# Optimization experiments

Measured on AMD Instinct MI355X. Metric: run time of the kernel, lower is better.

Reference implementation:

```python
import jax, jax.numpy as jnp
import numpy as np

N = 100_000   # nodes
E = 6_400_000  # edges (avg degree 64)
K = 3          # TAGConv hops -> K+1 linear terms per layer


def setup_inputs() -> dict:
    key = jax.random.key(0)
    ks = jax.random.split(key, 9)
    return {
        "x": jax.random.normal(ks[0], (N,), jnp.float32),
        "edge_index": jax.random.randint(ks[1], (2, E), 0, N, jnp.int32),
        "edge_attr": jax.random.normal(ks[2], (E,), jnp.float32),
        "k": 5000,
        "W1": jax.random.normal(ks[3], (K + 1, 1, 8), jnp.float32) * 0.5,
        "b1": jax.random.normal(ks[4], (8,), jnp.float32) * 0.1,
        "W2": jax.random.normal(ks[5], (K + 1, 8, 8), jnp.float32) * 0.2,
        "b2": jax.random.normal(ks[6], (8,), jnp.float32) * 0.1,
        "W3": jax.random.normal(ks[7], (K + 1, 8, 1), jnp.float32) * 0.2,
        "b3": jax.random.normal(ks[8], (1,), jnp.float32) * 0.1,
    }


def _gcn_norm(src, dst, edge_weight, num_nodes):
    # PyG gcn_norm with add_self_loops=False: deg over target index,
    # norm_e = d^{-1/2}[src] * w_e * d^{-1/2}[dst]
    deg = jax.ops.segment_sum(edge_weight, dst, num_segments=num_nodes)
    dis = jnp.where(deg > 0, jax.lax.rsqrt(jnp.where(deg > 0, deg, 1.0)), 0.0)
    return dis[src] * edge_weight * dis[dst]


def _tagconv(x, W, b, src, dst, norm, num_nodes):
    # out = sum_{h=0..K} (A_norm^h x) @ W[h] + b
    out = x @ W[0]
    h = x
    for i in range(1, W.shape[0]):
        h = jax.ops.segment_sum(norm[:, None] * h[src], dst, num_segments=num_nodes)
        out = out + h @ W[i]
    return out + b


def reference(x, edge_index, edge_attr, k, W1, b1, W2, b2, W3, b3):
    num_nodes = x.shape[0]
    x = x[:, None]  # [N, 1]
    src, dst = edge_index[0], edge_index[1]
    norm = _gcn_norm(src, dst, jnp.abs(edge_attr), num_nodes)

    x = jax.nn.relu(_tagconv(x, W1, b1, src, dst, norm, num_nodes))
    x = jax.nn.relu(_tagconv(x, W2, b2, src, dst, norm, num_nodes))
    x = jax.nn.relu(_tagconv(x, W3, b3, src, dst, norm, num_nodes))

    # tg.nn.InstanceNorm(1), batch=None, affine=False: normalize over all nodes
    mean = jnp.mean(x)
    var = jnp.mean((x - mean) ** 2)
    x = ((x - mean) * jax.lax.rsqrt(var + 1e-5)).squeeze(-1)  # [N]

    # top-k one-hot mask (argsort descending -> first k indices)
    _, top_idx = jax.lax.top_k(x, k)
    top_vec = jnp.zeros_like(x).at[top_idx].set(1.0)
    return jnp.column_stack((x, top_vec))  # [N, 2]
```

## Files before the change

### kernel.cpp

```cpp
#include <hip/hip_runtime.h>

#define BS 256
#define BSB 512
#define BSF 1024
#define GPN 16
#define NBLKB 1024
#define BSH 8
#define SMAX 400

static __device__ __forceinline__ float relu_(float v) { return fmaxf(v, 0.0f); }


__global__ void k_binhist(const int* __restrict__ dst, int* __restrict__ bcnt,
                          int E, int chunk, int nbuck) {
  __shared__ int h[1024];
  int b = blockIdx.x, t = threadIdx.x;
  for (int i = t; i < nbuck; i += BSB) h[i] = 0;
  __syncthreads();
  int beg = b * chunk, end = min(E, beg + chunk);
  for (int e = beg + t; e < end; e += BSB) atomicAdd(&h[dst[e] >> BSH], 1);
  __syncthreads();
  for (int i = t; i < nbuck; i += BSB) bcnt[(size_t)i * NBLKB + b] = h[i];
}

__global__ void k_bucketscan(int* __restrict__ bcnt, int* __restrict__ btot) {
  __shared__ int sh[BS];
  int bkt = blockIdx.x, t = threadIdx.x;
  size_t base = (size_t)bkt * NBLKB;
  int c[4], s = 0;
#pragma unroll
  for (int j = 0; j < 4; ++j) { c[j] = bcnt[base + t * 4 + j]; s += c[j]; }
  sh[t] = s; __syncthreads();
  for (int off = 1; off < BS; off <<= 1) {
    int add = (t >= off) ? sh[t - off] : 0; __syncthreads();
    sh[t] += add; __syncthreads();
  }
  int run = sh[t] - s;
#pragma unroll
  for (int j = 0; j < 4; ++j) { bcnt[base + t * 4 + j] = run; run += c[j]; }
  if (t == BS - 1) btot[bkt] = run;
}

__global__ void k_basescan(const int* __restrict__ btot, int* __restrict__ bbase, int nbuck) {
  __shared__ int sh[BS];
  int t = threadIdx.x;
  int run = 0;
  for (int c = 0; c < nbuck; c += BS) {
    int i = c + t;
    int v = (i < nbuck) ? btot[i] : 0;
    sh[t] = v; __syncthreads();
    for (int off = 1; off < BS; off <<= 1) {
      int add = (t >= off) ? sh[t - off] : 0; __syncthreads();
      sh[t] += add; __syncthreads();
    }
    if (i < nbuck) bbase[i] = run + sh[t] - v;
    run += sh[BS - 1];
    __syncthreads();
  }
}

__global__ void k_bin(const int* __restrict__ src, const int* __restrict__ dst,
                      const float* __restrict__ attr, const int* __restrict__ bcnt,
                      const int* __restrict__ bbase, int2* __restrict__ bed,
                      int E, int chunk, int nbuck) {
  __shared__ int2 stage[SMAX][9];
  __shared__ int  fc[SMAX];
  __shared__ int  cur[SMAX];
  int b = blockIdx.x, t = threadIdx.x;
  for (int i = t; i < nbuck; i += BSB) {
    cur[i] = bbase[i] + bcnt[(size_t)i * NBLKB + b];
    fc[i] = 0;
  }
  __syncthreads();
  int beg = b * chunk, end = min(E, beg + chunk);
  for (int base = beg; base < end; base += BSB) {
    int e = base + t;
    if (e < end) {
      int d = dst[e];
      int bkt = d >> BSH;
      int2 rec = make_int2((int)(((unsigned)(d & ((1 << BSH) - 1)) << 17) | (unsigned)src[e]),
                           __float_as_int(fabsf(attr[e])));
      int slot = atomicAdd(&fc[bkt], 1);
      if (slot < 8) stage[bkt][slot] = rec;
      else { int gp = atomicAdd(&cur[bkt], 1); bed[gp] = rec; }
    }
    __syncthreads();
    for (int i = t; i < nbuck; i += BSB) {
      int c = fc[i]; if (c > 8) c = 8;
      if (c == 8) {
        int gp = cur[i]; cur[i] = gp + 8;
#pragma unroll
        for (int j = 0; j < 8; ++j) bed[gp + j] = stage[i][j];
        fc[i] = 0;
      }
    }
    __syncthreads();
  }
  for (int i = t; i < nbuck; i += BSB) {
    int c = fc[i]; if (c > 8) c = 8;
    if (c) {
      int gp = cur[i];
      for (int j = 0; j < c; ++j) bed[gp + j] = stage[i][j];
    }
  }
}

__global__ void k_cntfill(const int2* __restrict__ bed, const int* __restrict__ bbase,
                          const int* __restrict__ btot, const float* __restrict__ x,
                          float* __restrict__ dis, float* __restrict__ xhat,
                          int* __restrict__ rowptr, int2* __restrict__ adj, int N, int E) {
  __shared__ int   lc[1 << BSH];
  __shared__ float ld[1 << BSH];
  __shared__ int   sc[1 << BSH];
  __shared__ int   rcur[1 << BSH];
  int bkt = blockIdx.x, t = threadIdx.x;
  if (t < (1 << BSH)) { lc[t] = 0; ld[t] = 0.f; }
  __syncthreads();
  int beg = bbase[bkt], tot = btot[bkt];
  for (int i = t; i < tot; i += BSF) {
    int2 rec = bed[beg + i];
    int dl = (int)((unsigned)rec.x >> 17);
    atomicAdd(&lc[dl], 1);
    atomicAdd(&ld[dl], __int_as_float(rec.y));
  }
  __syncthreads();
  if (t < (1 << BSH)) sc[t] = lc[t];
  __syncthreads();
  for (int off = 1; off < (1 << BSH); off <<= 1) {
    int add = 0;
    if (t < (1 << BSH) && t >= off) add = sc[t - off];
    __syncthreads();
    if (t < (1 << BSH)) sc[t] += add;
    __syncthreads();
  }
  if (t < (1 << BSH)) {
    int myrow = beg + sc[t] - lc[t];
    rcur[t] = myrow;
    int n = (bkt << BSH) + t;
    if (n < N) {
      rowptr[n] = myrow;
      float dg = ld[t];
      float d = (dg > 0.f) ? (1.0f / sqrtf(dg)) : 0.f;
      dis[n] = d;
      xhat[n] = d * x[n];
    }
  }
  if (bkt == (int)gridDim.x - 1 && t == 0) rowptr[N] = E;
  __syncthreads();
  for (int i = t; i < tot; i += BSF) {
    int2 rec = bed[beg + i];
    unsigned u = (unsigned)rec.x;
    int dl = (int)(u >> 17);
    int pos = atomicAdd(&rcur[dl], 1);
    adj[pos] = make_int2((int)(u & 0x1FFFFu), rec.y);
  }
}


__global__ void k_scanA(const int* __restrict__ cnt, int* __restrict__ bsum, int N) {
  __shared__ int sh[BS];
  int t = threadIdx.x;
  int base = blockIdx.x * 1024;
  int s = 0;
#pragma unroll
  for (int j = 0; j < 4; ++j) { int i = base + t * 4 + j; s += (i < N) ? cnt[i] : 0; }
  sh[t] = s; __syncthreads();
  for (int off = 128; off; off >>= 1) { if (t < off) sh[t] += sh[t + off]; __syncthreads(); }
  if (t == 0) bsum[blockIdx.x] = sh[0];
}

__global__ void k_scanB(int* __restrict__ bsum, int NB2) {
  __shared__ int sh[BS];
  int t = threadIdx.x;
  int v = (t < NB2) ? bsum[t] : 0;
  sh[t] = v; __syncthreads();
  for (int off = 1; off < BS; off <<= 1) {
    int add = (t >= off) ? sh[t - off] : 0; __syncthreads();
    sh[t] += add; __syncthreads();
  }
  if (t < NB2) bsum[t] = sh[t] - v;
}

__global__ void k_scanC(const int* __restrict__ cnt, const int* __restrict__ bsum,
                        int* __restrict__ rowptr, int* __restrict__ cursor, int N, int E) {
  __shared__ int sh[BS];
  int b = blockIdx.x, t = threadIdx.x;
  int base = b * 1024;
  int c[4]; int s = 0;
#pragma unroll
  for (int j = 0; j < 4; ++j) { int i = base + t * 4 + j; c[j] = (i < N) ? cnt[i] : 0; s += c[j]; }
  sh[t] = s; __syncthreads();
  for (int off = 1; off < BS; off <<= 1) {
    int add = (t >= off) ? sh[t - off] : 0; __syncthreads();
    sh[t] += add; __syncthreads();
  }
  int run = sh[t] - s + bsum[b];
#pragma unroll
  for (int j = 0; j < 4; ++j) {
    int i = base + t * 4 + j;
    if (i < N) { rowptr[i] = run; if (cursor) cursor[i] = run; run += c[j]; }
  }
  if (b == 0 && t == 0) rowptr[N] = E;
}

__global__ void k_count(const int* __restrict__ dst, int* __restrict__ cnt, int E) {
  int e = blockIdx.x * blockDim.x + threadIdx.x;
  if (e < E) atomicAdd(&cnt[dst[e]], 1);
}

__global__ void k_place(const int* __restrict__ src, const int* __restrict__ dst,
                        const float* __restrict__ attr, int* __restrict__ cursor,
                        int2* __restrict__ adj, int E) {
  int e = blockIdx.x * blockDim.x + threadIdx.x;
  if (e >= E) return;
  int d = dst[e];
  int pos = atomicAdd(&cursor[d], 1);
  adj[pos] = make_int2(src[e], __float_as_int(fabsf(attr[e])));
}

__global__ void k_degdis(const int* __restrict__ rowptr, const int2* __restrict__ adj,
                         const float* __restrict__ x, float* __restrict__ dis,
                         float* __restrict__ xhat, int N) {
  int g = (blockIdx.x * blockDim.x + threadIdx.x) / GPN;
  int l = threadIdx.x & (GPN - 1);
  if (g >= N) return;
  int beg = rowptr[g], end = rowptr[g + 1];
  float s = 0.0f;
  for (int e = beg + l; e < end; e += GPN) s += __int_as_float(adj[e].y);
#pragma unroll
  for (int off = 8; off; off >>= 1) s += __shfl_xor(s, off, GPN);
  if (l == 0) {
    float d = (s > 0.0f) ? (1.0f / sqrtf(s)) : 0.0f;
    dis[g] = d;
    xhat[g] = d * x[g];
  }
}


static __device__ __forceinline__ float edge_sum1(const int2* __restrict__ adj,
                                                  const float* __restrict__ uin,
                                                  int beg, int end, int l) {
  float a0 = 0.f, a1 = 0.f, a2 = 0.f, a3 = 0.f;
  int e = beg + l;
  for (; e + 3 * GPN < end; e += 4 * GPN) {
    int2 s0 = adj[e], s1 = adj[e + GPN], s2 = adj[e + 2 * GPN], s3 = adj[e + 3 * GPN];
    a0 += __int_as_float(s0.y) * uin[s0.x];
    a1 += __int_as_float(s1.y) * uin[s1.x];
    a2 += __int_as_float(s2.y) * uin[s2.x];
    a3 += __int_as_float(s3.y) * uin[s3.x];
  }
  for (; e < end; e += GPN) { int2 s0 = adj[e]; a0 += __int_as_float(s0.y) * uin[s0.x]; }
  float acc = (a0 + a1) + (a2 + a3);
#pragma unroll
  for (int off = 8; off; off >>= 1) acc += __shfl_xor(acc, off, GPN);
  return acc;
}

__global__ void k_gp1_uh(const int* __restrict__ rowptr, const int2* __restrict__ adj,
                         const float* __restrict__ uin, const float* __restrict__ dis,
                         float* __restrict__ hout, float* __restrict__ uout, int N) {
  int g = (blockIdx.x * blockDim.x + threadIdx.x) / GPN;
  int l = threadIdx.x & (GPN - 1);
  if (g >= N) return;
  float acc = edge_sum1(adj, uin, rowptr[g], rowptr[g + 1], l);
  if (l == 0) {
    float d = dis[g];
    float h = d * acc;
    hout[g] = h;
    uout[g] = d * h;
  }
}

__global__ void k_gp1_y(const int* __restrict__ rowptr, const int2* __restrict__ adj,
                        const float* __restrict__ u2, const float* __restrict__ x,
                        const float* __restrict__ h1, const float* __restrict__ h2,
                        const float* __restrict__ dis, const float* __restrict__ W1,
                        const float* __restrict__ b1, const float* __restrict__ W23,
                        float* __restrict__ y, float* __restrict__ Phat, int N) {
  int g = (blockIdx.x * blockDim.x + threadIdx.x) / GPN;
  int l = threadIdx.x & (GPN - 1);
  if (g >= N) return;
  float acc = edge_sum1(adj, u2, rowptr[g], rowptr[g + 1], l);
  if (l == 0) {
    float d = dis[g];
    float xv = x[g], a = h1[g], b = h2[g], c = d * acc;
    float o[8];
#pragma unroll
    for (int j = 0; j < 8; ++j)
      o[j] = relu_(xv * W1[j] + a * W1[8 + j] + b * W1[16 + j] + c * W1[24 + j] + b1[j]);
    float4* op = (float4*)(y + (size_t)g * 8);
    op[0] = make_float4(o[0], o[1], o[2], o[3]);
    op[1] = make_float4(o[4], o[5], o[6], o[7]);
    float p[8];
#pragma unroll
    for (int j = 0; j < 8; ++j) {
      float s = 0.0f;
#pragma unroll
      for (int i = 0; i < 8; ++i) s += o[i] * W23[i * 8 + j];
      p[j] = d * s;
    }
    float4* pp = (float4*)(Phat + (size_t)g * 8);
    pp[0] = make_float4(p[0], p[1], p[2], p[3]);
    pp[1] = make_float4(p[4], p[5], p[6], p[7]);
  }
}

#define EDGE_SUM8(ADJ, UIN, BEG, END, L)                                        \
  float a0=0,a1=0,a2=0,a3=0,a4=0,a5=0,a6=0,a7=0;                                \
  {                                                                             \
    int e = (BEG) + (L);                                                        \
    int last = (END) - GPN;                                                     \
    for (; e < last; e += 2 * GPN) {                                            \
      int2 s0 = (ADJ)[e], s1 = (ADJ)[e + GPN];                                  \
      float w0 = __int_as_float(s0.y), w1 = __int_as_float(s1.y);               \
      const float4* p0 = (const float4*)((UIN) + (size_t)s0.x * 8);             \
      const float4* p1 = (const float4*)((UIN) + (size_t)s1.x * 8);             \
      float4 u0 = p0[0], v0 = p0[1], u1 = p1[0], v1 = p1[1];                    \
      a0 += w0*u0.x; a1 += w0*u0.y; a2 += w0*u0.z; a3 += w0*u0.w;               \
      a4 += w0*v0.x; a5 += w0*v0.y; a6 += w0*v0.z; a7 += w0*v0.w;               \
      a0 += w1*u1.x; a1 += w1*u1.y; a2 += w1*u1.z; a3 += w1*u1.w;               \
      a4 += w1*v1.x; a5 += w1*v1.y; a6 += w1*v1.z; a7 += w1*v1.w;               \
    }                                                                           \
    if (e < (END)) {                                                            \
      int2 s0 = (ADJ)[e];                                                       \
      float w0 = __int_as_float(s0.y);                                          \
      const float4* p0 = (const float4*)((UIN) + (size_t)s0.x * 8);             \
      float4 u0 = p0[0], v0 = p0[1];                                            \
      a0 += w0*u0.x; a1 += w0*u0.y; a2 += w0*u0.z; a3 += w0*u0.w;               \
      a4 += w0*v0.x; a5 += w0*v0.y; a6 += w0*v0.z; a7 += w0*v0.w;               \
    }                                                                           \
  }                                                                             \
  _Pragma("unroll")                                                             \
  for (int off = 8; off; off >>= 1) {                                           \
    a0 += __shfl_xor(a0, off, GPN); a1 += __shfl_xor(a1, off, GPN);             \
    a2 += __shfl_xor(a2, off, GPN); a3 += __shfl_xor(a3, off, GPN);             \
    a4 += __shfl_xor(a4, off, GPN); a5 += __shfl_xor(a5, off, GPN);             \
    a6 += __shfl_xor(a6, off, GPN); a7 += __shfl_xor(a7, off, GPN);             \
  }

__global__ void k_gp8_u(const int* __restrict__ rowptr, const int2* __restrict__ adj,
                        const float* __restrict__ uin, const float* __restrict__ y,
                        const float* __restrict__ W, const float* __restrict__ dis,
                        float* __restrict__ uout, int N) {
  int g = (blockIdx.x * blockDim.x + threadIdx.x) / GPN;
  int l = threadIdx.x & (GPN - 1);
  if (g >= N) return;
  int beg = rowptr[g], end = rowptr[g + 1];
  EDGE_SUM8(adj, uin, beg, end, l)
  if (l == 0) {
    float d = dis[g];
    const float4* yp = (const float4*)(y + (size_t)g * 8);
    float4 u = yp[0], v = yp[1];
    float yi[8] = {u.x, u.y, u.z, u.w, v.x, v.y, v.z, v.w};
    float acc[8] = {a0, a1, a2, a3, a4, a5, a6, a7};
    float o[8];
#pragma unroll
    for (int j = 0; j < 8; ++j) {
      float s = 0.0f;
#pragma unroll
      for (int i = 0; i < 8; ++i) s += yi[i] * W[i * 8 + j];
      o[j] = d * (s + d * acc[j]);
    }
    float4* op = (float4*)(uout + (size_t)g * 8);
    op[0] = make_float4(o[0], o[1], o[2], o[3]);
    op[1] = make_float4(o[4], o[5], o[6], o[7]);
  }
}

__global__ void k_gp8_fin(const int* __restrict__ rowptr, const int2* __restrict__ adj,
                          const float* __restrict__ uin, const float* __restrict__ y,
                          const float* __restrict__ W0, const float* __restrict__ b2,
                          const float* __restrict__ W3, const float* __restrict__ dis,
                          float* __restrict__ S3hat, float* __restrict__ B2,
                          float* __restrict__ B1, float* __restrict__ B0, int N) {
  int g = (blockIdx.x * blockDim.x + threadIdx.x) / GPN;
  int l = threadIdx.x & (GPN - 1);
  if (g >= N) return;
  int beg = rowptr[g], end = rowptr[g + 1];
  EDGE_SUM8(adj, uin, beg, end, l)
  if (l == 0) {
    float d = dis[g];
    const float4* yp = (const float4*)(y + (size_t)g * 8);
    float4 u = yp[0], v = yp[1];
    float yi[8] = {u.x, u.y, u.z, u.w, v.x, v.y, v.z, v.w};
    float acc[8] = {a0, a1, a2, a3, a4, a5, a6, a7};
    float z[8];
#pragma unroll
    for (int j = 0; j < 8; ++j) {
      float s = 0.0f;
#pragma unroll
      for (int i = 0; i < 8; ++i) s += yi[i] * W0[i * 8 + j];
      z[j] = relu_(s + d * acc[j] + b2[j]);
    }
    float tt[4];
#pragma unroll
    for (int i = 0; i < 4; ++i) {
      float s = 0.0f;
#pragma unroll
      for (int j = 0; j < 8; ++j) s += z[j] * W3[i * 8 + j];
      tt[i] = s;
    }
    B0[g] = tt[0]; B1[g] = tt[1]; B2[g] = tt[2];
    S3hat[g] = d * tt[3];
  }
}

__global__ void k_gp1_bu(const int* __restrict__ rowptr, const int2* __restrict__ adj,
                         const float* __restrict__ uin, const float* __restrict__ B,
                         const float* __restrict__ dis, float* __restrict__ uout, int N) {
  int g = (blockIdx.x * blockDim.x + threadIdx.x) / GPN;
  int l = threadIdx.x & (GPN - 1);
  if (g >= N) return;
  float acc = edge_sum1(adj, uin, rowptr[g], rowptr[g + 1], l);
  if (l == 0) {
    float d = dis[g];
    uout[g] = d * (B[g] + d * acc);
  }
}

__global__ void k_gp1_last(const int* __restrict__ rowptr, const int2* __restrict__ adj,
                           const float* __restrict__ uin, const float* __restrict__ B0,
                           const float* __restrict__ b3, const float* __restrict__ dis,
                           float* __restrict__ r, unsigned* __restrict__ keys,
                           double* __restrict__ partials, int N) {
  __shared__ double s1[BS];
  __shared__ double s2[BS];
  int tid = blockIdx.x * blockDim.x + threadIdx.x;
  int g = tid / GPN, l = tid & (GPN - 1);
  float rv = 0.0f;
  bool writer = false;
  if (g < N) {
    float acc = edge_sum1(adj, uin, rowptr[g], rowptr[g + 1], l);
    if (l == 0) {
      float gg = B0[g] + dis[g] * acc;
      rv = relu_(gg + b3[0]);
      r[g] = rv;
      keys[g] = __float_as_uint(rv) | 0x80000000u;
      writer = true;
    }
  }
  double v = writer ? (double)rv : 0.0;
  s1[threadIdx.x] = v;
  s2[threadIdx.x] = v * v;
  __syncthreads();
  for (int off = 128; off; off >>= 1) {
    if (threadIdx.x < off) {
      s1[threadIdx.x] += s1[threadIdx.x + off];
      s2[threadIdx.x] += s2[threadIdx.x + off];
    }
    __syncthreads();
  }
  if (threadIdx.x == 0) {
    partials[2 * (size_t)blockIdx.x]     = s1[0];
    partials[2 * (size_t)blockIdx.x + 1] = s2[0];
  }
}

__global__ void k_stats(const double* __restrict__ partials, int nparts,
                        float* __restrict__ stats, unsigned* __restrict__ state,
                        const int* __restrict__ kp, int N) {
  __shared__ double s1[BS];
  __shared__ double s2[BS];
  int t = threadIdx.x;
  double a = 0.0, b = 0.0;
  for (int i = t; i < nparts; i += BS) { a += partials[2 * (size_t)i]; b += partials[2 * (size_t)i + 1]; }
  s1[t] = a; s2[t] = b;
  __syncthreads();
  for (int off = 128; off; off >>= 1) {
    if (t < off) { s1[t] += s1[t + off]; s2[t] += s2[t + off]; }
    __syncthreads();
  }
  if (t == 0) {
    double mean = s1[0] / (double)N;
    double var  = s2[0] / (double)N - mean * mean;
    stats[0] = (float)mean;
    stats[1] = (float)(1.0 / sqrt(var + 1e-5));
    state[0] = 0u;
    state[1] = (unsigned)kp[0];
  }
}


__global__ void k_hist(const unsigned* __restrict__ keys, int N,
                       const unsigned* __restrict__ state, unsigned* __restrict__ hist,
                       int shift) {
  __shared__ unsigned sh[256];
  sh[threadIdx.x] = 0;
  __syncthreads();
  unsigned prefix = state[0];
  unsigned hmask = (shift >= 24) ? 0u : (0xFFFFFFFFu << (shift + 8));
  int stride = gridDim.x * blockDim.x;
  for (int n = blockIdx.x * blockDim.x + threadIdx.x; n < N; n += stride) {
    unsigned kk = keys[n];
    if ((kk & hmask) == (prefix & hmask)) atomicAdd(&sh[(kk >> shift) & 255u], 1u);
  }
  __syncthreads();
  atomicAdd(&hist[threadIdx.x], sh[threadIdx.x]);
}

__global__ void k_select(unsigned* __restrict__ state, unsigned* __restrict__ hist, int shift) {
  __shared__ unsigned sh[BS];
  int t = threadIdx.x;
  unsigned c = hist[t];
  sh[t] = c;
  __syncthreads();
  for (int off = 1; off < BS; off <<= 1) {
    unsigned add = (t + off < BS) ? sh[t + off] : 0u; __syncthreads();
    sh[t] += add; __syncthreads();
  }
  unsigned rem = state[1];
  unsigned S = sh[t];
  if (S >= rem && (S - c) < rem) {
    state[0] |= ((unsigned)t) << shift;
    state[1] = rem - (S - c);
  }
  hist[t] = 0;
}

__global__ void k_mark(const unsigned* __restrict__ keys, const float* __restrict__ r,
                       const float* __restrict__ stats, int N,
                       const unsigned* __restrict__ state, float* __restrict__ out,
                       unsigned* __restrict__ blkcnt) {
  unsigned T = state[0];
  float mean = stats[0], istd = stats[1];
  int n = blockIdx.x * 256 + threadIdx.x;
  int eq = 0;
  __shared__ int sh;
  if (threadIdx.x == 0) sh = 0;
  __syncthreads();
  if (n < N) {
    out[2 * (size_t)n] = (r[n] - mean) * istd;
    unsigned kk = keys[n];
    out[2 * (size_t)n + 1] = (kk > T) ? 1.0f : 0.0f;
    eq = (kk == T);
  }
  if (eq) atomicAdd(&sh, 1);
  __syncthreads();
  if (threadIdx.x == 0) blkcnt[blockIdx.x] = (unsigned)sh;
}

__global__ void k_scanP(const unsigned* __restrict__ blkcnt, unsigned* __restrict__ scanbuf, int NB) {
  __shared__ unsigned sh[BS];
  int t = threadIdx.x;
  unsigned c0 = (2 * t < NB) ? blkcnt[2 * t] : 0u;
  unsigned c1 = (2 * t + 1 < NB) ? blkcnt[2 * t + 1] : 0u;
  unsigned s = c0 + c1;
  sh[t] = s; __syncthreads();
  for (int off = 1; off < BS; off <<= 1) {
    unsigned add = (t >= off) ? sh[t - off] : 0u; __syncthreads();
    sh[t] += add; __syncthreads();
  }
  unsigned ex = sh[t] - s;
  if (2 * t < NB) scanbuf[2 * t] = ex;
  if (2 * t + 1 < NB) scanbuf[2 * t + 1] = ex + c0;
}

__global__ void k_resolve(const unsigned* __restrict__ keys, int N,
                          const unsigned* __restrict__ state,
                          const unsigned* __restrict__ scanbuf, float* __restrict__ out) {
  unsigned T = state[0];
  unsigned m = state[1];
  int n = blockIdx.x * 256 + threadIdx.x;
  if (n >= N) return;
  if (keys[n] != T) return;
  unsigned rank = scanbuf[blockIdx.x];
  int base = blockIdx.x * 256;
  for (int j = base; j < n; ++j) rank += (keys[j] == T);
  out[2 * (size_t)n + 1] = (rank < m) ? 1.0f : 0.0f;
}


extern "C" void kernel_launch(void* const* d_in, const int* in_sizes, int n_in,
                              void* d_out, int out_size, void* d_ws, size_t ws_size,
                              hipStream_t stream) {
  const float* x    = (const float*)d_in[0];
  const int*   ei   = (const int*)d_in[1];
  const float* attr = (const float*)d_in[2];
  const int*   kp   = (const int*)d_in[3];
  const float* W1   = (const float*)d_in[4];
  const float* b1   = (const float*)d_in[5];
  const float* W2   = (const float*)d_in[6];
  const float* b2   = (const float*)d_in[7];
  const float* W3   = (const float*)d_in[8];
  const float* b3   = (const float*)d_in[9];
  const int N = in_sizes[0];
  const int E = in_sizes[2];
  const int* src = ei;
  const int* dst = ei + E;
  float* out = (float*)d_out;
  const int NB    = (N + 255) / 256;
  const int NB2   = (N + 1023) / 1024;
  const int NBUCK = (N + (1 << BSH) - 1) >> BSH;
  const int chunk = (E + NBLKB - 1) / NBLKB;
  const int GGB   = (int)(((size_t)N * GPN + BS - 1) / BS);

  char* p = (char*)d_ws;
  auto alloc = [&](size_t bytes) -> char* {
    char* r = p; p += (bytes + 255) & ~(size_t)255; return r;
  };
  float*    dis    = (float*)alloc((size_t)N * 4);
  float*    xhat   = (float*)alloc((size_t)N * 4);
  float*    h1     = (float*)alloc((size_t)N * 4);
  float*    h2     = (float*)alloc((size_t)N * 4);
  float*    u1     = (float*)alloc((size_t)N * 4);
  float*    u2     = (float*)alloc((size_t)N * 4);
  float*    y      = (float*)alloc((size_t)N * 32);
  float*    Phat   = (float*)alloc((size_t)N * 32);
  float*    Qhat   = (float*)alloc((size_t)N * 32);
  float*    S3hat  = (float*)alloc((size_t)N * 4);
  float*    B2     = (float*)alloc((size_t)N * 4);
  float*    B1     = (float*)alloc((size_t)N * 4);
  float*    B0     = (float*)alloc((size_t)N * 4);
  float*    g2hat  = (float*)alloc((size_t)N * 4);
  float*    g1hat  = (float*)alloc((size_t)N * 4);
  float*    r      = (float*)alloc((size_t)N * 4);
  unsigned* keys   = (unsigned*)alloc((size_t)N * 4);
  double*   parts  = (double*)alloc((size_t)GGB * 16);
  float*    stats  = (float*)alloc(8);
  unsigned* state  = (unsigned*)alloc(8);
  unsigned* hist   = (unsigned*)alloc(1024);
  unsigned* blkcnt = (unsigned*)alloc((size_t)NB * 4);
  unsigned* scanbf = (unsigned*)alloc((size_t)NB * 4);
  int*      rowptr = (int*)alloc((size_t)(N + 1) * 4);
  int*      cursor = (int*)alloc((size_t)N * 4);
  int*      cnt    = (int*)alloc((size_t)N * 4);
  int*      bsum   = (int*)alloc(2048);
  int2*     adj    = (int2*)alloc((size_t)E * 8);
  int2*     bed    = (int2*)alloc((size_t)E * 8);
  int*      bcnt   = (int*)alloc((size_t)NBUCK * NBLKB * 4);
  int*      btot   = (int*)alloc((size_t)NBUCK * 4 + 256);
  int*      bbase  = (int*)alloc((size_t)NBUCK * 4 + 256);
  size_t need_new = (size_t)(p - (char*)d_ws);

  dim3 B(BS);
  int genb = (E + BS - 1) / BS;
  dim3 GE(genb), GG(GGB), GN(NB), GB(NBUCK);

  bool use_new = (need_new <= ws_size) && (N <= 102400) && (NBUCK <= SMAX);

  hipMemsetAsync(hist, 0, 1024, stream);

  if (use_new) {
    k_binhist<<<dim3(NBLKB), dim3(BSB), 0, stream>>>(dst, bcnt, E, chunk, NBUCK);
    k_bucketscan<<<GB, B, 0, stream>>>(bcnt, btot);
    k_basescan<<<dim3(1), B, 0, stream>>>(btot, bbase, NBUCK);
    k_bin<<<dim3(NBLKB), dim3(BSB), 0, stream>>>(src, dst, attr, bcnt, bbase, bed, E, chunk, NBUCK);
    k_cntfill<<<GB, dim3(BSF), 0, stream>>>(bed, bbase, btot, x, dis, xhat, rowptr, adj, N, E);
  } else {
    hipMemsetAsync(cnt, 0, (size_t)N * 4, stream);
    k_count<<<GE, B, 0, stream>>>(dst, cnt, E);
    k_scanA<<<dim3(NB2), B, 0, stream>>>(cnt, bsum, N);
    k_scanB<<<dim3(1), B, 0, stream>>>(bsum, NB2);
    k_scanC<<<dim3(NB2), B, 0, stream>>>(cnt, bsum, rowptr, cursor, N, E);
    k_place<<<GE, B, 0, stream>>>(src, dst, attr, cursor, adj, E);
    k_degdis<<<GG, B, 0, stream>>>(rowptr, adj, x, dis, xhat, N);
  }

  k_gp1_uh<<<GG, B, 0, stream>>>(rowptr, adj, xhat, dis, h1, u1, N);
  k_gp1_uh<<<GG, B, 0, stream>>>(rowptr, adj, u1, dis, h2, u2, N);
  k_gp1_y<<<GG, B, 0, stream>>>(rowptr, adj, u2, x, h1, h2, dis, W1, b1, W2 + 3 * 64, y, Phat, N);

  k_gp8_u<<<GG, B, 0, stream>>>(rowptr, adj, Phat, y, W2 + 2 * 64, dis, Qhat, N);
  k_gp8_u<<<GG, B, 0, stream>>>(rowptr, adj, Qhat, y, W2 + 1 * 64, dis, Phat, N);
  k_gp8_fin<<<GG, B, 0, stream>>>(rowptr, adj, Phat, y, W2, b2, W3, dis, S3hat, B2, B1, B0, N);

  k_gp1_bu<<<GG, B, 0, stream>>>(rowptr, adj, S3hat, B2, dis, g2hat, N);
  k_gp1_bu<<<GG, B, 0, stream>>>(rowptr, adj, g2hat, B1, dis, g1hat, N);
  k_gp1_last<<<GG, B, 0, stream>>>(rowptr, adj, g1hat, B0, b3, dis, r, keys, parts, N);

  k_stats<<<dim3(1), B, 0, stream>>>(parts, GGB, stats, state, kp, N);

  for (int shift = 24; shift >= 0; shift -= 8) {
    k_hist<<<GN, B, 0, stream>>>(keys, N, state, hist, shift);
    k_select<<<dim3(1), B, 0, stream>>>(state, hist, shift);
  }
  k_mark<<<GN, B, 0, stream>>>(keys, r, stats, N, state, out, blkcnt);
  k_scanP<<<dim3(1), B, 0, stream>>>(blkcnt, scanbf, NB);
  k_resolve<<<GN, B, 0, stream>>>(keys, N, state, scanbf, out);
}
```

Baseline: 539.7 us.

## Run graph propagations directly on bucketed edge lists with shared-memory atomics

```diff
diff --git a/kernel.cpp b/kernel.cpp
--- a/kernel.cpp
+++ b/kernel.cpp
@@ -6,6 +6,7 @@
 #define GPN 16
 #define NBLKB 1024
 #define BSH 8
+#define NPB (1 << BSH)
 #define SMAX 400
 
 static __device__ __forceinline__ float relu_(float v) { return fmaxf(v, 0.0f); }
@@ -78,7 +79,7 @@
     if (e < end) {
       int d = dst[e];
       int bkt = d >> BSH;
-      int2 rec = make_int2((int)(((unsigned)(d & ((1 << BSH) - 1)) << 17) | (unsigned)src[e]),
+      int2 rec = make_int2((int)(((unsigned)(d & (NPB - 1)) << 17) | (unsigned)src[e]),
                            __float_as_int(fabsf(attr[e])));
       int slot = atomicAdd(&fc[bkt], 1);
       if (slot < 8) stage[bkt][slot] = rec;
@@ -105,54 +106,249 @@
   }
 }
 
-__global__ void k_cntfill(const int2* __restrict__ bed, const int* __restrict__ bbase,
+__global__ void kb_degdis(const int2* __restrict__ bed, const int* __restrict__ bbase,
                           const int* __restrict__ btot, const float* __restrict__ x,
-                          float* __restrict__ dis, float* __restrict__ xhat,
-                          int* __restrict__ rowptr, int2* __restrict__ adj, int N, int E) {
-  __shared__ int   lc[1 << BSH];
-  __shared__ float ld[1 << BSH];
-  __shared__ int   sc[1 << BSH];
-  __shared__ int   rcur[1 << BSH];
+                          float* __restrict__ dis, float* __restrict__ xhat, int N) {
+  __shared__ float ld[NPB];
   int bkt = blockIdx.x, t = threadIdx.x;
-  if (t < (1 << BSH)) { lc[t] = 0; ld[t] = 0.f; }
+  if (t < NPB) ld[t] = 0.f;
   __syncthreads();
   int beg = bbase[bkt], tot = btot[bkt];
   for (int i = t; i < tot; i += BSF) {
     int2 rec = bed[beg + i];
-    int dl = (int)((unsigned)rec.x >> 17);
-    atomicAdd(&lc[dl], 1);
-    atomicAdd(&ld[dl], __int_as_float(rec.y));
-  }
-  __syncthreads();
-  if (t < (1 << BSH)) sc[t] = lc[t];
-  __syncthreads();
-  for (int off = 1; off < (1 << BSH); off <<= 1) {
-    int add = 0;
-    if (t < (1 << BSH) && t >= off) add = sc[t - off];
-    __syncthreads();
-    if (t < (1 << BSH)) sc[t] += add;
-    __syncthreads();
-  }
-  if (t < (1 << BSH)) {
-    int myrow = beg + sc[t] - lc[t];
-    rcur[t] = myrow;
+    atomicAdd(&ld[(unsigned)rec.x >> 17], __int_as_float(rec.y));
+  }
+  __syncthreads();
+  if (t < NPB) {
     int n = (bkt << BSH) + t;
     if (n < N) {
-      rowptr[n] = myrow;
       float dg = ld[t];
       float d = (dg > 0.f) ? (1.0f / sqrtf(dg)) : 0.f;
       dis[n] = d;
       xhat[n] = d * x[n];
     }
   }
-  if (bkt == (int)gridDim.x - 1 && t == 0) rowptr[N] = E;
-  __syncthreads();
+}
+
+
+__global__ void kb_gp1_uh(const int2* __restrict__ bed, const int* __restrict__ bbase,
+                          const int* __restrict__ btot, const float* __restrict__ uin,
+                          const float* __restrict__ dis, float* __restrict__ hout,
+                          float* __restrict__ uout, int N) {
+  __shared__ float acc[NPB];
+  int bkt = blockIdx.x, t = threadIdx.x;
+  if (t < NPB) acc[t] = 0.f;
+  __syncthreads();
+  int beg = bbase[bkt], tot = btot[bkt];
   for (int i = t; i < tot; i += BSF) {
     int2 rec = bed[beg + i];
     unsigned u = (unsigned)rec.x;
-    int dl = (int)(u >> 17);
-    int pos = atomicAdd(&rcur[dl], 1);
-    adj[pos] = make_int2((int)(u & 0x1FFFFu), rec.y);
+    atomicAdd(&acc[u >> 17], __int_as_float(rec.y) * uin[u & 0x1FFFFu]);
+  }
+  __syncthreads();
+  if (t < NPB) {
+    int n = (bkt << BSH) + t;
+    if (n < N) {
+      float d = dis[n];
+      float h = d * acc[t];
+      hout[n] = h;
+      uout[n] = d * h;
+    }
+  }
+}
+
+__global__ void kb_gp1_y(const int2* __restrict__ bed, const int* __restrict__ bbase,
+                         const int* __restrict__ btot, const float* __restrict__ u2,
+                         const float* __restrict__ x, const float* __restrict__ h1,
+                         const float* __restrict__ h2, const float* __restrict__ dis,
+                         const float* __restrict__ W1, const float* __restrict__ b1,
+                         const float* __restrict__ W23, float* __restrict__ y,
+                         float* __restrict__ Phat, int N) {
+  __shared__ float acc[NPB];
+  int bkt = blockIdx.x, t = threadIdx.x;
+  if (t < NPB) acc[t] = 0.f;
+  __syncthreads();
+  int beg = bbase[bkt], tot = btot[bkt];
+  for (int i = t; i < tot; i += BSF) {
+    int2 rec = bed[beg + i];
+    unsigned u = (unsigned)rec.x;
+    atomicAdd(&acc[u >> 17], __int_as_float(rec.y) * u2[u & 0x1FFFFu]);
+  }
+  __syncthreads();
+  if (t < NPB) {
+    int n = (bkt << BSH) + t;
+    if (n < N) {
+      float d = dis[n];
+      float xv = x[n], a = h1[n], b = h2[n], c = d * acc[t];
+      float o[8];
+#pragma unroll
+      for (int j = 0; j < 8; ++j)
+        o[j] = relu_(xv * W1[j] + a * W1[8 + j] + b * W1[16 + j] + c * W1[24 + j] + b1[j]);
+      float4* op = (float4*)(y + (size_t)n * 8);
+      op[0] = make_float4(o[0], o[1], o[2], o[3]);
+      op[1] = make_float4(o[4], o[5], o[6], o[7]);
+      float pv[8];
+#pragma unroll
+      for (int j = 0; j < 8; ++j) {
+        float s = 0.0f;
+#pragma unroll
+        for (int i2 = 0; i2 < 8; ++i2) s += o[i2] * W23[i2 * 8 + j];
+        pv[j] = d * s;
+      }
+      float4* pp = (float4*)(Phat + (size_t)n * 8);
+      pp[0] = make_float4(pv[0], pv[1], pv[2], pv[3]);
+      pp[1] = make_float4(pv[4], pv[5], pv[6], pv[7]);
+    }
+  }
+}
+
+#define KB8_STREAM(UIN)                                                          \
+  __shared__ float acc[NPB][9];                                                  \
+  int bkt = blockIdx.x, t = threadIdx.x;                                         \
+  for (int i = t; i < NPB * 9; i += BSF) ((float*)acc)[i] = 0.f;                 \
+  __syncthreads();                                                               \
+  int beg = bbase[bkt], tot = btot[bkt];                                         \
+  for (int i = t; i < tot; i += BSF) {                                           \
+    int2 rec = bed[beg + i];                                                     \
+    unsigned u = (unsigned)rec.x;                                                \
+    int dl = (int)(u >> 17), s = (int)(u & 0x1FFFFu);                            \
+    float w = __int_as_float(rec.y);                                             \
+    const float4* hp = (const float4*)((UIN) + (size_t)s * 8);                   \
+    float4 a = hp[0], b = hp[1];                                                 \
+    atomicAdd(&acc[dl][0], w * a.x); atomicAdd(&acc[dl][1], w * a.y);            \
+    atomicAdd(&acc[dl][2], w * a.z); atomicAdd(&acc[dl][3], w * a.w);            \
+    atomicAdd(&acc[dl][4], w * b.x); atomicAdd(&acc[dl][5], w * b.y);            \
+    atomicAdd(&acc[dl][6], w * b.z); atomicAdd(&acc[dl][7], w * b.w);            \
+  }                                                                              \
+  __syncthreads();
+
+__global__ void kb_gp8_u(const int2* __restrict__ bed, const int* __restrict__ bbase,
+                         const int* __restrict__ btot, const float* __restrict__ uin,
+                         const float* __restrict__ y, const float* __restrict__ W,
+                         const float* __restrict__ dis, float* __restrict__ uout, int N) {
+  KB8_STREAM(uin)
+  if (t < NPB) {
+    int n = (bkt << BSH) + t;
+    if (n < N) {
+      float d = dis[n];
+      const float4* yp = (const float4*)(y + (size_t)n * 8);
+      float4 u = yp[0], v = yp[1];
+      float yi[8] = {u.x, u.y, u.z, u.w, v.x, v.y, v.z, v.w};
+      float o[8];
+#pragma unroll
+      for (int j = 0; j < 8; ++j) {
+        float s = 0.0f;
+#pragma unroll
+        for (int i2 = 0; i2 < 8; ++i2) s += yi[i2] * W[i2 * 8 + j];
+        o[j] = d * (s + d * acc[t][j]);
+      }
+      float4* op = (float4*)(uout + (size_t)n * 8);
+      op[0] = make_float4(o[0], o[1], o[2], o[3]);
+      op[1] = make_float4(o[4], o[5], o[6], o[7]);
+    }
+  }
+}
+
+__global__ void kb_gp8_fin(const int2* __restrict__ bed, const int* __restrict__ bbase,
+                           const int* __restrict__ btot, const float* __restrict__ uin,
+                           const float* __restrict__ y, const float* __restrict__ W0,
+                           const float* __restrict__ b2, const float* __restrict__ W3,
+                           const float* __restrict__ dis, float* __restrict__ S3hat,
+                           float* __restrict__ B2, float* __restrict__ B1,
+                           float* __restrict__ B0, int N) {
+  KB8_STREAM(uin)
+  if (t < NPB) {
+    int n = (bkt << BSH) + t;
+    if (n < N) {
+      float d = dis[n];
+      const float4* yp = (const float4*)(y + (size_t)n * 8);
+      float4 u = yp[0], v = yp[1];
+      float yi[8] = {u.x, u.y, u.z, u.w, v.x, v.y, v.z, v.w};
+      float z[8];
+#pragma unroll
+      for (int j = 0; j < 8; ++j) {
+        float s = 0.0f;
+#pragma unroll
+        for (int i2 = 0; i2 < 8; ++i2) s += yi[i2] * W0[i2 * 8 + j];
+        z[j] = relu_(s + d * acc[t][j] + b2[j]);
+      }
+      float tt[4];
+#pragma unroll
+      for (int i2 = 0; i2 < 4; ++i2) {
+        float s = 0.0f;
+#pragma unroll
+        for (int j = 0; j < 8; ++j) s += z[j] * W3[i2 * 8 + j];
+        tt[i2] = s;
+      }
+      B0[n] = tt[0]; B1[n] = tt[1]; B2[n] = tt[2];
+      S3hat[n] = d * tt[3];
+    }
+  }
+}
+
+__global__ void kb_gp1_bu(const int2* __restrict__ bed, const int* __restrict__ bbase,
+                          const int* __restrict__ btot, const float* __restrict__ uin,
+                          const float* __restrict__ B, const float* __restrict__ dis,
+                          float* __restrict__ uout, int N) {
+  __shared__ float acc[NPB];
+  int bkt = blockIdx.x, t = threadIdx.x;
+  if (t < NPB) acc[t] = 0.f;
+  __syncthreads();
+  int beg = bbase[bkt], tot = btot[bkt];
+  for (int i = t; i < tot; i += BSF) {
+    int2 rec = bed[beg + i];
+    unsigned u = (unsigned)rec.x;
+    atomicAdd(&acc[u >> 17], __int_as_float(rec.y) * uin[u & 0x1FFFFu]);
+  }
+  __syncthreads();
+  if (t < NPB) {
+    int n = (bkt << BSH) + t;
+    if (n < N) {
+      float d = dis[n];
+      uout[n] = d * (B[n] + d * acc[t]);
+    }
+  }
+}
+
+__global__ void kb_gp1_last(const int2* __restrict__ bed, const int* __restrict__ bbase,
+                            const int* __restrict__ btot, const float* __restrict__ uin,
+                            const float* __restrict__ B0, const float* __restrict__ b3,
+                            const float* __restrict__ dis, float* __restrict__ r,
+                            unsigned* __restrict__ keys, double* __restrict__ partials, int N) {
+  __shared__ float acc[NPB];
+  __shared__ double s1[BSF];
+  __shared__ double s2[BSF];
+  int bkt = blockIdx.x, t = threadIdx.x;
+  if (t < NPB) acc[t] = 0.f;
+  __syncthreads();
+  int beg = bbase[bkt], tot = btot[bkt];
+  for (int i = t; i < tot; i += BSF) {
+    int2 rec = bed[beg + i];
+    unsigned u = (unsigned)rec.x;
+    atomicAdd(&acc[u >> 17], __int_as_float(rec.y) * uin[u & 0x1FFFFu]);
+  }
+  __syncthreads();
+  double v = 0.0;
+  if (t < NPB) {
+    int n = (bkt << BSH) + t;
+    if (n < N) {
+      float d = dis[n];
+      float rv = relu_(B0[n] + d * acc[t] + b3[0]);
+      r[n] = rv;
+      keys[n] = __float_as_uint(rv) | 0x80000000u;
+      v = (double)rv;
+    }
+  }
+  s1[t] = v;
+  s2[t] = v * v;
+  __syncthreads();
+  for (int off = BSF / 2; off; off >>= 1) {
+    if (t < off) { s1[t] += s1[t + off]; s2[t] += s2[t + off]; }
+    __syncthreads();
+  }
+  if (t == 0) {
+    partials[2 * (size_t)bkt]     = s1[0];
+    partials[2 * (size_t)bkt + 1] = s2[0];
   }
 }
 
@@ -236,21 +432,19 @@
   }
 }
 
-
 static __device__ __forceinline__ float edge_sum1(const int2* __restrict__ adj,
                                                   const float* __restrict__ uin,
                                                   int beg, int end, int l) {
-  float a0 = 0.f, a1 = 0.f, a2 = 0.f, a3 = 0.f;
+  float acc0 = 0.0f, acc1 = 0.0f;
   int e = beg + l;
-  for (; e + 3 * GPN < end; e += 4 * GPN) {
-    int2 s0 = adj[e], s1 = adj[e + GPN], s2 = adj[e + 2 * GPN], s3 = adj[e + 3 * GPN];
-    a0 += __int_as_float(s0.y) * uin[s0.x];
-    a1 += __int_as_float(s1.y) * uin[s1.x];
-    a2 += __int_as_float(s2.y) * uin[s2.x];
-    a3 += __int_as_float(s3.y) * uin[s3.x];
-  }
-  for (; e < end; e += GPN) { int2 s0 = adj[e]; a0 += __int_as_float(s0.y) * uin[s0.x]; }
-  float acc = (a0 + a1) + (a2 + a3);
+  int last = end - GPN;
+  for (; e < last; e += 2 * GPN) {
+    int2 s0 = adj[e], s1 = adj[e + GPN];
+    acc0 += __int_as_float(s0.y) * uin[s0.x];
+    acc1 += __int_as_float(s1.y) * uin[s1.x];
+  }
+  if (e < end) { int2 s0 = adj[e]; acc0 += __int_as_float(s0.y) * uin[s0.x]; }
+  float acc = acc0 + acc1;
 #pragma unroll
   for (int off = 8; off; off >>= 1) acc += __shfl_xor(acc, off, GPN);
   return acc;
@@ -590,7 +784,7 @@
   float* out = (float*)d_out;
   const int NB    = (N + 255) / 256;
   const int NB2   = (N + 1023) / 1024;
-  const int NBUCK = (N + (1 << BSH) - 1) >> BSH;
+  const int NBUCK = (N + NPB - 1) >> BSH;
   const int chunk = (E + NBLKB - 1) / NBLKB;
   const int GGB   = (int)(((size_t)N * GPN + BS - 1) / BS);
 
@@ -645,7 +839,19 @@
     k_bucketscan<<<GB, B, 0, stream>>>(bcnt, btot);
     k_basescan<<<dim3(1), B, 0, stream>>>(btot, bbase, NBUCK);
     k_bin<<<dim3(NBLKB), dim3(BSB), 0, stream>>>(src, dst, attr, bcnt, bbase, bed, E, chunk, NBUCK);
-    k_cntfill<<<GB, dim3(BSF), 0, stream>>>(bed, bbase, btot, x, dis, xhat, rowptr, adj, N, E);
+    kb_degdis<<<GB, dim3(BSF), 0, stream>>>(bed, bbase, btot, x, dis, xhat, N);
+
+    kb_gp1_uh<<<GB, dim3(BSF), 0, stream>>>(bed, bbase, btot, xhat, dis, h1, u1, N);
+    kb_gp1_uh<<<GB, dim3(BSF), 0, stream>>>(bed, bbase, btot, u1, dis, h2, u2, N);
+    kb_gp1_y<<<GB, dim3(BSF), 0, stream>>>(bed, bbase, btot, u2, x, h1, h2, dis, W1, b1, W2 + 3 * 64, y, Phat, N);
+    kb_gp8_u<<<GB, dim3(BSF), 0, stream>>>(bed, bbase, btot, Phat, y, W2 + 2 * 64, dis, Qhat, N);
+    kb_gp8_u<<<GB, dim3(BSF), 0, stream>>>(bed, bbase, btot, Qhat, y, W2 + 1 * 64, dis, Phat, N);
+    kb_gp8_fin<<<GB, dim3(BSF), 0, stream>>>(bed, bbase, btot, Phat, y, W2, b2, W3, dis, S3hat, B2, B1, B0, N);
+    kb_gp1_bu<<<GB, dim3(BSF), 0, stream>>>(bed, bbase, btot, S3hat, B2, dis, g2hat, N);
+    kb_gp1_bu<<<GB, dim3(BSF), 0, stream>>>(bed, bbase, btot, g2hat, B1, dis, g1hat, N);
+    kb_gp1_last<<<GB, dim3(BSF), 0, stream>>>(bed, bbase, btot, g1hat, B0, b3, dis, r, keys, parts, N);
+
+    k_stats<<<dim3(1), B, 0, stream>>>(parts, NBUCK, stats, state, kp, N);
   } else {
     hipMemsetAsync(cnt, 0, (size_t)N * 4, stream);
     k_count<<<GE, B, 0, stream>>>(dst, cnt, E);
@@ -654,21 +860,19 @@
     k_scanC<<<dim3(NB2), B, 0, stream>>>(cnt, bsum, rowptr, cursor, N, E);
     k_place<<<GE, B, 0, stream>>>(src, dst, attr, cursor, adj, E);
     k_degdis<<<GG, B, 0, stream>>>(rowptr, adj, x, dis, xhat, N);
-  }
-
-  k_gp1_uh<<<GG, B, 0, stream>>>(rowptr, adj, xhat, dis, h1, u1, N);
-  k_gp1_uh<<<GG, B, 0, stream>>>(rowptr, adj, u1, dis, h2, u2, N);
-  k_gp1_y<<<GG, B, 0, stream>>>(rowptr, adj, u2, x, h1, h2, dis, W1, b1, W2 + 3 * 64, y, Phat, N);
-
-  k_gp8_u<<<GG, B, 0, stream>>>(rowptr, adj, Phat, y, W2 + 2 * 64, dis, Qhat, N);
-  k_gp8_u<<<GG, B, 0, stream>>>(rowptr, adj, Qhat, y, W2 + 1 * 64, dis, Phat, N);
-  k_gp8_fin<<<GG, B, 0, stream>>>(rowptr, adj, Phat, y, W2, b2, W3, dis, S3hat, B2, B1, B0, N);
-
-  k_gp1_bu<<<GG, B, 0, stream>>>(rowptr, adj, S3hat, B2, dis, g2hat, N);
-  k_gp1_bu<<<GG, B, 0, stream>>>(rowptr, adj, g2hat, B1, dis, g1hat, N);
-  k_gp1_last<<<GG, B, 0, stream>>>(rowptr, adj, g1hat, B0, b3, dis, r, keys, parts, N);
-
-  k_stats<<<dim3(1), B, 0, stream>>>(parts, GGB, stats, state, kp, N);
+
+    k_gp1_uh<<<GG, B, 0, stream>>>(rowptr, adj, xhat, dis, h1, u1, N);
+    k_gp1_uh<<<GG, B, 0, stream>>>(rowptr, adj, u1, dis, h2, u2, N);
+    k_gp1_y<<<GG, B, 0, stream>>>(rowptr, adj, u2, x, h1, h2, dis, W1, b1, W2 + 3 * 64, y, Phat, N);
+    k_gp8_u<<<GG, B, 0, stream>>>(rowptr, adj, Phat, y, W2 + 2 * 64, dis, Qhat, N);
+    k_gp8_u<<<GG, B, 0, stream>>>(rowptr, adj, Qhat, y, W2 + 1 * 64, dis, Phat, N);
+    k_gp8_fin<<<GG, B, 0, stream>>>(rowptr, adj, Phat, y, W2, b2, W3, dis, S3hat, B2, B1, B0, N);
+    k_gp1_bu<<<GG, B, 0, stream>>>(rowptr, adj, S3hat, B2, dis, g2hat, N);
+    k_gp1_bu<<<GG, B, 0, stream>>>(rowptr, adj, g2hat, B1, dis, g1hat, N);
+    k_gp1_last<<<GG, B, 0, stream>>>(rowptr, adj, g1hat, B0, b3, dis, r, keys, parts, N);
+
+    k_stats<<<dim3(1), B, 0, stream>>>(parts, GGB, stats, state, kp, N);
+  }
 
   for (int shift = 24; shift >= 0; shift -= 8) {
     k_hist<<<GN, B, 0, stream>>>(keys, N, state, hist, shift);
```

New measurement: 1.460 ms. 2.71x slower.
